# Performance work log

Hardware: AMD Instinct MI355X
Metric: run time of the kernel (lower is better)

## Reference

```python
import jax, jax.numpy as jnp
import numpy as np

D_MODEL = 1024
D_STATE = 16
EXPAND = 2
D_CONV = 4
D_INNER = EXPAND * D_MODEL
BATCH = 1
SEQLEN = 2048


def setup_inputs() -> dict:
    key = jax.random.key(0)
    ks = jax.random.split(key, 8)
    s = 0.02
    x = jax.random.normal(ks[0], (BATCH, SEQLEN, D_MODEL), jnp.float32)
    W_in = jax.random.normal(ks[1], (2 * D_INNER, D_MODEL), jnp.float32) * s
    conv_w = jax.random.normal(ks[2], (D_INNER, 1, D_CONV), jnp.float32) * s
    conv_b = jnp.zeros((D_INNER,), jnp.float32)
    # A_log init as in module: log(arange(1, d_state+1)) tiled over d_inner
    A_log = jnp.log(jnp.tile(jnp.arange(1, D_STATE + 1, dtype=jnp.float32), (D_INNER, 1)))
    D_param = jnp.ones((D_INNER,), jnp.float32)
    W_x = jax.random.normal(ks[3], (2 * D_STATE, D_INNER), jnp.float32) * s
    W_dt = jax.random.normal(ks[4], (D_INNER, D_INNER), jnp.float32) * s
    b_dt = jnp.zeros((D_INNER,), jnp.float32)
    W_out = jax.random.normal(ks[5], (D_MODEL, D_INNER), jnp.float32) * s
    return {"x": x, "W_in": W_in, "conv_w": conv_w, "conv_b": conv_b,
            "A_log": A_log, "D_param": D_param, "W_x": W_x,
            "W_dt": W_dt, "b_dt": b_dt, "W_out": W_out}


def reference(x, W_in, conv_w, conv_b, A_log, D_param, W_x, W_dt, b_dt, W_out):
    B_, L, _ = x.shape
    xz = jnp.einsum('bld,ed->ble', x, W_in)          # [B,L,2*d_inner]
    x_inner, z = jnp.split(xz, 2, axis=-1)
    # causal depthwise conv1d (pad left d_conv-1 == torch pad-both + slice[:L])
    xc = jax.lax.conv_general_dilated(
        jnp.swapaxes(x_inner, 1, 2), conv_w, (1,), [(D_CONV - 1, 0)],
        feature_group_count=D_INNER,
        dimension_numbers=('NCH', 'OIH', 'NCH')) + conv_b[None, :, None]
    x_ssm = jnp.swapaxes(jax.nn.silu(xc), 1, 2)       # [B,L,d_inner]
    dt = jax.nn.softplus(jnp.einsum('ble,fe->blf', x_ssm, W_dt) + b_dt)
    x_dbl = jnp.einsum('ble,se->bls', x_ssm, W_x)     # [B,L,2*d_state]
    B_mat, C_mat = jnp.split(x_dbl, 2, axis=-1)       # each [B,L,d_state]
    A = -jnp.exp(A_log)                               # [d_inner,d_state]
    dA = jnp.exp(dt[..., None] * A)                   # [B,L,d_inner,d_state]
    dBx = B_mat[:, :, None, :] * dt[..., None] * x_ssm[..., None]

    def step(h, inp):
        dA_t, dBx_t, C_t = inp
        h = dA_t * h + dBx_t                          # [B,d_inner,d_state]
        y_t = jnp.einsum('bds,bs->bd', h, C_t)
        return h, y_t

    h0 = jnp.zeros((B_, D_INNER, D_STATE), x.dtype)
    _, ys = jax.lax.scan(step, h0, (jnp.swapaxes(dA, 0, 1),
                                    jnp.swapaxes(dBx, 0, 1),
                                    jnp.swapaxes(C_mat, 0, 1)))
    y = jnp.swapaxes(ys, 0, 1) + D_param * x_ssm      # [B,L,d_inner]
    y = y * jax.nn.silu(z)
    out = jnp.einsum('ble,de->bld', y, W_out)
    return out + x
```

## Files before the change

### kernel.cpp

```cpp
#include <hip/hip_runtime.h>

#define L_SEQ 2048
#define DMODEL 1024
#define DINNER 2048
#define NCHUNK 128
#define TCHUNK 16

typedef __attribute__((ext_vector_type(8))) short bf16x8;
typedef __attribute__((ext_vector_type(4))) float f32x4;

__device__ __forceinline__ float bf2f(unsigned short u) {
  return __uint_as_float(((unsigned)u) << 16);
}
__device__ __forceinline__ unsigned short f2bf(float f) {
  unsigned u = __float_as_uint(f);
  return (unsigned short)((u + 0x7FFFu + ((u >> 16) & 1u)) >> 16);
}
__device__ __forceinline__ void gload_lds16(const void* g, void* l) {
  __builtin_amdgcn_global_load_lds(
      (const __attribute__((address_space(1))) void*)g,
      (__attribute__((address_space(3))) void*)l, 16, 0, 0);
}

__global__ void cvt_f32_bf16(const float4* __restrict__ in, ushort4* __restrict__ out, int n4) {
  int i = blockIdx.x * blockDim.x + threadIdx.x;
  if (i >= n4) return;
  float4 v = in[i];
  ushort4 o;
  o.x = f2bf(v.x); o.y = f2bf(v.y); o.z = f2bf(v.z); o.w = f2bf(v.w);
  out[i] = o;
}

__global__ void zero_bf16(ushort4* __restrict__ out, int n4) {
  int i = blockIdx.x * blockDim.x + threadIdx.x;
  if (i >= n4) return;
  out[i] = ushort4{0, 0, 0, 0};
}

template <int EPI>
__global__ __launch_bounds__(256) void gemm_bt3(
    const unsigned short* __restrict__ A, const unsigned short* __restrict__ B,
    int M, int N, int K, int nx, int ksplit,
    float* __restrict__ outf, unsigned short* __restrict__ outb,
    const float* __restrict__ aux) {
  __shared__ __align__(16) unsigned short As[3 * 128 * 32];
  __shared__ __align__(16) unsigned short Bs[3 * 128 * 32];
  const int tid = threadIdx.x;
  const int lane = tid & 63;
  const int wave = tid >> 6;
  const int wm = wave >> 1, wn = wave & 1;

  const int nwg = gridDim.x;
  const int wg = blockIdx.x;
  const int swzb = (wg & 7) * (nwg >> 3) + (wg >> 3);
  const int tiles = nwg / ksplit;
  const int ks = swzb / tiles;
  const int t = swzb - ks * tiles;
  const int bx = t % nx, by = t / nx;
  const int bm = by * 128, bn = bx * 128;
  const int Ks = K / ksplit;
  const int kbeg = ks * Ks;
  const int nk = Ks >> 5;

  const int srow = tid >> 2, sc4 = tid & 3;
  const int scp = sc4 ^ ((srow >> 1) & 3);
  const unsigned short* Ag = A + (size_t)(bm + srow) * K + scp * 8;
  const unsigned short* Bg = B + (size_t)(bn + srow) * K + scp * 8;
  unsigned short* AsW = &As[srow * 32 + sc4 * 8];
  unsigned short* BsW = &Bs[srow * 32 + sc4 * 8];

  auto STAGE = [&](int buf, int k0) {
    gload_lds16(Ag + k0, AsW + buf * 4096);
    gload_lds16(Ag + (size_t)64 * K + k0, AsW + buf * 4096 + 64 * 32);
    gload_lds16(Bg + k0, BsW + buf * 4096);
    gload_lds16(Bg + (size_t)64 * K + k0, BsW + buf * 4096 + 64 * 32);
  };

  f32x4 acc[4][4] = {};

  const int g = lane >> 4;
  const int r16 = lane & 15;
  const int sw = (g ^ ((r16 >> 1) & 3)) * 8;

  STAGE(0, kbeg);
  STAGE(1, kbeg + 32);
  int cur = 0, stg = 2;

  for (int i = 0; i < nk; ++i) {
    if (i < nk - 1) {
      asm volatile("s_waitcnt vmcnt(4)" ::: "memory");
    } else {
      asm volatile("s_waitcnt vmcnt(0)" ::: "memory");
    }
    __builtin_amdgcn_s_barrier();
    asm volatile("" ::: "memory");
    if (i + 2 < nk) {
      STAGE(stg, kbeg + (i + 2) * 32);
      stg = (stg == 2) ? 0 : stg + 1;
    }

    bf16x8 a[4], b[4];
#pragma unroll
    for (int ii = 0; ii < 4; ++ii)
      a[ii] = *(const bf16x8*)&As[cur * 4096 + (wm * 64 + ii * 16 + r16) * 32 + sw];
#pragma unroll
    for (int j = 0; j < 4; ++j)
      b[j] = *(const bf16x8*)&Bs[cur * 4096 + (wn * 64 + j * 16 + r16) * 32 + sw];
#pragma unroll
    for (int ii = 0; ii < 4; ++ii)
#pragma unroll
      for (int j = 0; j < 4; ++j)
        acc[ii][j] = __builtin_amdgcn_mfma_f32_16x16x32_bf16(a[ii], b[j], acc[ii][j], 0, 0, 0);

    cur = (cur == 2) ? 0 : cur + 1;
  }

  const int rq = lane >> 4;
#pragma unroll
  for (int i = 0; i < 4; ++i)
#pragma unroll
    for (int j = 0; j < 4; ++j)
#pragma unroll
      for (int r = 0; r < 4; ++r) {
        int row = bm + wm * 64 + i * 16 + rq * 4 + r;
        int col = bn + wn * 64 + j * 16 + r16;
        float v = acc[i][j][r];
        if (EPI == 0) {
          outb[(size_t)row * N + col] = f2bf(v);
        } else if (EPI == 3) {
          if (col < 2048) {
            float tt = v + aux[col];
            float sp = (tt > 15.f) ? tt : log1pf(__expf(tt));
            outb[(size_t)row * 2048 + col] = f2bf(sp);
          } else if (col < 2080) {
            outf[(size_t)row * 32 + (col - 2048)] = v;
          }
        } else {
          outf[(size_t)ks * M * N + (size_t)row * N + col] = v;
        }
      }
}

__global__ void reduce_addx(const float4* __restrict__ p, const float4* __restrict__ x,
                            float4* __restrict__ out, int n4) {
  int i = blockIdx.x * 256 + threadIdx.x;
  if (i >= n4) return;
  float4 a = p[i], b = p[n4 + i], c = x[i];
  float4 o;
  o.x = a.x + b.x + c.x; o.y = a.y + b.y + c.y;
  o.z = a.z + b.z + c.z; o.w = a.w + b.w + c.w;
  out[i] = o;
}

__global__ __launch_bounds__(256) void conv_silu8(
    const unsigned short* __restrict__ xz,
    const float* __restrict__ cw, const float* __restrict__ cb,
    unsigned short* __restrict__ x_ssm, unsigned short* __restrict__ sz_out) {
  int idx = blockIdx.x * 256 + threadIdx.x;
  int l = idx >> 8, c0 = (idx & 255) * 8;
  float acc[8];
  float4 b0 = *(const float4*)(cb + c0);
  float4 b1 = *(const float4*)(cb + c0 + 4);
  acc[0] = b0.x; acc[1] = b0.y; acc[2] = b0.z; acc[3] = b0.w;
  acc[4] = b1.x; acc[5] = b1.y; acc[6] = b1.z; acc[7] = b1.w;
  float4 w[8];
#pragma unroll
  for (int j = 0; j < 8; ++j) w[j] = *(const float4*)(cw + (c0 + j) * 4);
#pragma unroll
  for (int k = 0; k < 4; ++k) {
    int lt = l - 3 + k;
    if (lt >= 0) {
      bf16x8 v = *(const bf16x8*)(xz + (size_t)lt * 4096 + c0);
      const float* wk = (const float*)w;
#pragma unroll
      for (int j = 0; j < 8; ++j)
        acc[j] = fmaf(bf2f((unsigned short)v[j]), wk[j * 4 + k], acc[j]);
    }
  }
  bf16x8 zr = *(const bf16x8*)(xz + (size_t)l * 4096 + 2048 + c0);
  bf16x8 ox, oz;
#pragma unroll
  for (int j = 0; j < 8; ++j) {
    float a = acc[j];
    ox[j] = (short)f2bf(a / (1.f + __expf(-a)));
    float zv = bf2f((unsigned short)zr[j]);
    oz[j] = (short)f2bf(zv / (1.f + __expf(-zv)));
  }
  *(bf16x8*)(x_ssm + (size_t)idx * 8) = ox;
  *(bf16x8*)(sz_out + (size_t)idx * 8) = oz;
}

__global__ __launch_bounds__(256) void scan_passA(
    const unsigned short* __restrict__ dtb, const unsigned short* __restrict__ x_ssm,
    const float* __restrict__ x_dbl, const float* __restrict__ A_log,
    float* __restrict__ Pout, float* __restrict__ Hout) {
  int tid = threadIdx.x;
  int c = blockIdx.x & (NCHUNK - 1), db = blockIdx.x >> 7;
  int d = db * 256 + tid;
  int t0 = c * TCHUNK;
  float Av[16];
  const float4* al4 = (const float4*)(A_log + d * 16);
#pragma unroll
  for (int q = 0; q < 4; ++q) {
    float4 a = al4[q];
    Av[q * 4 + 0] = -__expf(a.x); Av[q * 4 + 1] = -__expf(a.y);
    Av[q * 4 + 2] = -__expf(a.z); Av[q * 4 + 3] = -__expf(a.w);
  }
  float h[16];
#pragma unroll
  for (int s = 0; s < 16; ++s) h[s] = 0.f;
  float sum_dt = 0.f;
#pragma unroll 2
  for (int i = 0; i < TCHUNK; ++i) {
    int t = t0 + i;
    float dtv = bf2f(dtb[(size_t)t * 2048 + d]);
    float xv = bf2f(x_ssm[(size_t)t * 2048 + d]);
    float dtx = dtv * xv;
    sum_dt += dtv;
    const float* B = x_dbl + t * 32;
#pragma unroll
    for (int s = 0; s < 16; ++s) {
      float dA = __expf(dtv * Av[s]);
      h[s] = fmaf(dA, h[s], B[s] * dtx);
    }
  }
  float* Ho = Hout + (size_t)c * 32768 + d * 16;
  float* Po = Pout + (size_t)c * 32768 + d * 16;
#pragma unroll
  for (int s = 0; s < 16; ++s) Ho[s] = h[s];
#pragma unroll
  for (int s = 0; s < 16; ++s) Po[s] = __expf(sum_dt * Av[s]);
}

__global__ __launch_bounds__(256) void scan_passB(
    float* __restrict__ P, const float* __restrict__ Hloc) {
  int i = blockIdx.x * 256 + threadIdx.x;
  float h = 0.f;
  for (int c = 0; c < NCHUNK; ++c) {
    size_t o = (size_t)c * 32768 + i;
    float p = P[o];
    float hl = Hloc[o];
    P[o] = h;
    h = fmaf(p, h, hl);
  }
}

__global__ __launch_bounds__(256) void scan_passC(
    const unsigned short* __restrict__ dtb, const unsigned short* __restrict__ x_ssm,
    const float* __restrict__ x_dbl, const float* __restrict__ A_log,
    const float* __restrict__ D_param, const unsigned short* __restrict__ silu_z,
    const float* __restrict__ Hinit, unsigned short* __restrict__ y_out) {
  int tid = threadIdx.x;
  int c = blockIdx.x & (NCHUNK - 1), db = blockIdx.x >> 7;
  int d = db * 256 + tid;
  int t0 = c * TCHUNK;
  float Av[16];
  const float4* al4 = (const float4*)(A_log + d * 16);
#pragma unroll
  for (int q = 0; q < 4; ++q) {
    float4 a = al4[q];
    Av[q * 4 + 0] = -__expf(a.x); Av[q * 4 + 1] = -__expf(a.y);
    Av[q * 4 + 2] = -__expf(a.z); Av[q * 4 + 3] = -__expf(a.w);
  }
  float Dp = D_param[d];
  float h[16];
  const float4* hi4 = (const float4*)(Hinit + (size_t)c * 32768 + d * 16);
#pragma unroll
  for (int q = 0; q < 4; ++q) {
    float4 v = hi4[q];
    h[q * 4 + 0] = v.x; h[q * 4 + 1] = v.y; h[q * 4 + 2] = v.z; h[q * 4 + 3] = v.w;
  }
#pragma unroll 2
  for (int i = 0; i < TCHUNK; ++i) {
    int t = t0 + i;
    float dtv = bf2f(dtb[(size_t)t * 2048 + d]);
    float xv = bf2f(x_ssm[(size_t)t * 2048 + d]);
    float dtx = dtv * xv;
    const float* B = x_dbl + t * 32;
    const float* C = x_dbl + t * 32 + 16;
    float y = 0.f;
#pragma unroll
    for (int s = 0; s < 16; ++s) {
      float dA = __expf(dtv * Av[s]);
      h[s] = fmaf(dA, h[s], B[s] * dtx);
      y = fmaf(h[s], C[s], y);
    }
    float szv = bf2f(silu_z[(size_t)t * 2048 + d]);
    y_out[(size_t)t * 2048 + d] = f2bf((y + Dp * xv) * szv);
  }
}

extern "C" void kernel_launch(void* const* d_in, const int* in_sizes, int n_in,
                              void* d_out, int out_size, void* d_ws, size_t ws_size,
                              hipStream_t stream) {
  const float* x      = (const float*)d_in[0];
  const float* W_in   = (const float*)d_in[1];
  const float* conv_w = (const float*)d_in[2];
  const float* conv_b = (const float*)d_in[3];
  const float* A_log  = (const float*)d_in[4];
  const float* D_par  = (const float*)d_in[5];
  const float* W_x    = (const float*)d_in[6];
  const float* W_dt   = (const float*)d_in[7];
  const float* b_dt   = (const float*)d_in[8];
  const float* W_out  = (const float*)d_in[9];
  float* out = (float*)d_out;

  char* ws = (char*)d_ws;
  unsigned short* xbf    = (unsigned short*)(ws + 0);
  unsigned short* Winbf  = (unsigned short*)(ws + ((size_t)4 << 20));
  unsigned short* Wcomb  = (unsigned short*)(ws + ((size_t)12 << 20));
  unsigned short* Woutbf = (unsigned short*)(ws + ((size_t)21 << 20));
  unsigned short* xz     = (unsigned short*)(ws + ((size_t)25 << 20));
  unsigned short* xssm   = (unsigned short*)(ws + ((size_t)41 << 20));
  unsigned short* siluz  = (unsigned short*)(ws + ((size_t)49 << 20));
  unsigned short* dtb    = (unsigned short*)(ws + ((size_t)57 << 20));
  float* xdbl            = (float*)(ws + ((size_t)65 << 20));
  unsigned short* yfin   = (unsigned short*)(ws + ((size_t)66 << 20));
  float* Pbuf            = (float*)(ws + ((size_t)25 << 20));
  float* Hloc            = (float*)(ws + ((size_t)4 << 20));
  float* part            = (float*)(ws + ((size_t)41 << 20));

  cvt_f32_bf16<<<2048, 256, 0, stream>>>((const float4*)x, (ushort4*)xbf, (L_SEQ * DMODEL) / 4);
  cvt_f32_bf16<<<4096, 256, 0, stream>>>((const float4*)W_in, (ushort4*)Winbf, (2 * DINNER * DMODEL) / 4);
  cvt_f32_bf16<<<4096, 256, 0, stream>>>((const float4*)W_dt, (ushort4*)Wcomb, (DINNER * DINNER) / 4);
  cvt_f32_bf16<<<64, 256, 0, stream>>>((const float4*)W_x, (ushort4*)(Wcomb + (size_t)2048 * 2048),
                                       (32 * DINNER) / 4);
  zero_bf16<<<192, 256, 0, stream>>>((ushort4*)(Wcomb + (size_t)2080 * 2048), (96 * DINNER) / 4);
  cvt_f32_bf16<<<2048, 256, 0, stream>>>((const float4*)W_out, (ushort4*)Woutbf, (DMODEL * DINNER) / 4);

  gemm_bt3<0><<<512, 256, 0, stream>>>(xbf, Winbf, L_SEQ, 4096, DMODEL, 32, 1,
                                       nullptr, xz, nullptr);

  conv_silu8<<<2048, 256, 0, stream>>>(xz, conv_w, conv_b, xssm, siluz);

  gemm_bt3<3><<<272, 256, 0, stream>>>(xssm, Wcomb, L_SEQ, 2176, DINNER, 17, 1,
                                       xdbl, dtb, b_dt);

  scan_passA<<<NCHUNK * (DINNER / 256), 256, 0, stream>>>(dtb, xssm, xdbl, A_log, Pbuf, Hloc);
  scan_passB<<<(DINNER * 16) / 256, 256, 0, stream>>>(Pbuf, Hloc);
  scan_passC<<<NCHUNK * (DINNER / 256), 256, 0, stream>>>(dtb, xssm, xdbl, A_log, D_par, siluz,
                                                          Pbuf, yfin);

  gemm_bt3<4><<<256, 256, 0, stream>>>(yfin, Woutbf, L_SEQ, DMODEL, DINNER, 8, 2,
                                       part, nullptr, nullptr);
  reduce_addx<<<(L_SEQ * DMODEL / 4 + 255) / 256, 256, 0, stream>>>(
      (const float4*)part, (const float4*)x, (float4*)out, L_SEQ * DMODEL / 4);
}
```

Measured before the change: 320.0 us.

## Deepen GEMM K-tile to 64 with 4-stage pipeline and halve scan chunk count

The bf16 GEMM now stages 128x64 K-tiles through a 4-buffer LDS ring with three loads in flight, using an 8-slot XOR swizzle and two MFMA sub-steps per barrier. This halves the number of barriers and waitcnt points per K and deepens prefetch. LDS use grows from 48KB to 128KB per block, which likely limits occupancy to one block per CU. Separately, the chunked scan uses 64 chunks of 32 timesteps instead of 128 of 16, cutting the serial pass-B length and the P/H traffic but giving the parallel passes fewer blocks.

```diff
diff --git a/kernel.cpp b/kernel.cpp
--- a/kernel.cpp
+++ b/kernel.cpp
@@ -3,8 +3,8 @@
 #define L_SEQ 2048
 #define DMODEL 1024
 #define DINNER 2048
-#define NCHUNK 128
-#define TCHUNK 16
+#define NCHUNK 64
+#define TCHUNK 32
 
 typedef __attribute__((ext_vector_type(8))) short bf16x8;
 typedef __attribute__((ext_vector_type(4))) float f32x4;
@@ -38,13 +38,13 @@
 }
 
 template <int EPI>
-__global__ __launch_bounds__(256) void gemm_bt3(
+__global__ __launch_bounds__(256) void gemm_bk64(
     const unsigned short* __restrict__ A, const unsigned short* __restrict__ B,
     int M, int N, int K, int nx, int ksplit,
     float* __restrict__ outf, unsigned short* __restrict__ outb,
     const float* __restrict__ aux) {
-  __shared__ __align__(16) unsigned short As[3 * 128 * 32];
-  __shared__ __align__(16) unsigned short Bs[3 * 128 * 32];
+  __shared__ __align__(16) unsigned short As[4 * 128 * 64];
+  __shared__ __align__(16) unsigned short Bs[4 * 128 * 64];
   const int tid = threadIdx.x;
   const int lane = tid & 63;
   const int wave = tid >> 6;
@@ -60,59 +60,67 @@
   const int bm = by * 128, bn = bx * 128;
   const int Ks = K / ksplit;
   const int kbeg = ks * Ks;
-  const int nk = Ks >> 5;
-
-  const int srow = tid >> 2, sc4 = tid & 3;
-  const int scp = sc4 ^ ((srow >> 1) & 3);
-  const unsigned short* Ag = A + (size_t)(bm + srow) * K + scp * 8;
-  const unsigned short* Bg = B + (size_t)(bn + srow) * K + scp * 8;
-  unsigned short* AsW = &As[srow * 32 + sc4 * 8];
-  unsigned short* BsW = &Bs[srow * 32 + sc4 * 8];
-
-  auto STAGE = [&](int buf, int k0) {
-    gload_lds16(Ag + k0, AsW + buf * 4096);
-    gload_lds16(Ag + (size_t)64 * K + k0, AsW + buf * 4096 + 64 * 32);
-    gload_lds16(Bg + k0, BsW + buf * 4096);
-    gload_lds16(Bg + (size_t)64 * K + k0, BsW + buf * 4096 + 64 * 32);
+  const int nst = Ks >> 6;
+
+  const int srow = wave * 8 + (lane >> 3);
+  const int swslot = (lane & 7) ^ ((lane >> 3) & 7);
+  const unsigned short* Ag = A + (size_t)(bm + srow) * K + kbeg + swslot * 8;
+  const unsigned short* Bg = B + (size_t)(bn + srow) * K + kbeg + swslot * 8;
+
+  auto STAGE = [&](int buf, int kof) {
+#pragma unroll
+    for (int q = 0; q < 4; ++q) {
+      gload_lds16(Ag + (size_t)q * 32 * K + kof, &As[buf * 8192 + (q * 32 + wave * 8) * 64]);
+      gload_lds16(Bg + (size_t)q * 32 * K + kof, &Bs[buf * 8192 + (q * 32 + wave * 8) * 64]);
+    }
   };
 
   f32x4 acc[4][4] = {};
 
   const int g = lane >> 4;
   const int r16 = lane & 15;
-  const int sw = (g ^ ((r16 >> 1) & 3)) * 8;
-
-  STAGE(0, kbeg);
-  STAGE(1, kbeg + 32);
-  int cur = 0, stg = 2;
-
-  for (int i = 0; i < nk; ++i) {
-    if (i < nk - 1) {
-      asm volatile("s_waitcnt vmcnt(4)" ::: "memory");
+  const int rsw = r16 & 7;
+
+  STAGE(0, 0);
+  STAGE(1, 64);
+  STAGE(2, 128);
+  int cur = 0, stg = 3;
+
+  for (int i = 0; i < nst; ++i) {
+    int rem = nst - 1 - i;
+    if (rem >= 2) {
+      asm volatile("s_waitcnt vmcnt(16)" ::: "memory");
+    } else if (rem == 1) {
+      asm volatile("s_waitcnt vmcnt(8)" ::: "memory");
     } else {
       asm volatile("s_waitcnt vmcnt(0)" ::: "memory");
     }
     __builtin_amdgcn_s_barrier();
     asm volatile("" ::: "memory");
-    if (i + 2 < nk) {
-      STAGE(stg, kbeg + (i + 2) * 32);
-      stg = (stg == 2) ? 0 : stg + 1;
-    }
-
-    bf16x8 a[4], b[4];
-#pragma unroll
-    for (int ii = 0; ii < 4; ++ii)
-      a[ii] = *(const bf16x8*)&As[cur * 4096 + (wm * 64 + ii * 16 + r16) * 32 + sw];
-#pragma unroll
-    for (int j = 0; j < 4; ++j)
-      b[j] = *(const bf16x8*)&Bs[cur * 4096 + (wn * 64 + j * 16 + r16) * 32 + sw];
-#pragma unroll
-    for (int ii = 0; ii < 4; ++ii)
+    if (i + 3 < nst) {
+      STAGE(stg, (i + 3) * 64);
+      stg = (stg + 1) & 3;
+    }
+
+#pragma unroll
+    for (int kk = 0; kk < 2; ++kk) {
+      bf16x8 a[4], b[4];
+#pragma unroll
+      for (int ii = 0; ii < 4; ++ii)
+        a[ii] = *(const bf16x8*)&As[cur * 8192 + (wm * 64 + ii * 16 + r16) * 64 +
+                                    ((kk * 4 + g) ^ rsw) * 8];
 #pragma unroll
       for (int j = 0; j < 4; ++j)
-        acc[ii][j] = __builtin_amdgcn_mfma_f32_16x16x32_bf16(a[ii], b[j], acc[ii][j], 0, 0, 0);
-
-    cur = (cur == 2) ? 0 : cur + 1;
+        b[j] = *(const bf16x8*)&Bs[cur * 8192 + (wn * 64 + j * 16 + r16) * 64 +
+                                   ((kk * 4 + g) ^ rsw) * 8];
+#pragma unroll
+      for (int ii = 0; ii < 4; ++ii)
+#pragma unroll
+        for (int j = 0; j < 4; ++j)
+          acc[ii][j] = __builtin_amdgcn_mfma_f32_16x16x32_bf16(a[ii], b[j], acc[ii][j], 0, 0, 0);
+    }
+
+    cur = (cur + 1) & 3;
   }
 
   const int rq = lane >> 4;
@@ -195,7 +203,7 @@
     const float* __restrict__ x_dbl, const float* __restrict__ A_log,
     float* __restrict__ Pout, float* __restrict__ Hout) {
   int tid = threadIdx.x;
-  int c = blockIdx.x & (NCHUNK - 1), db = blockIdx.x >> 7;
+  int c = blockIdx.x & (NCHUNK - 1), db = blockIdx.x / NCHUNK;
   int d = db * 256 + tid;
   int t0 = c * TCHUNK;
   float Av[16];
@@ -251,7 +259,7 @@
     const float* __restrict__ D_param, const unsigned short* __restrict__ silu_z,
     const float* __restrict__ Hinit, unsigned short* __restrict__ y_out) {
   int tid = threadIdx.x;
-  int c = blockIdx.x & (NCHUNK - 1), db = blockIdx.x >> 7;
+  int c = blockIdx.x & (NCHUNK - 1), db = blockIdx.x / NCHUNK;
   int d = db * 256 + tid;
   int t0 = c * TCHUNK;
   float Av[16];
@@ -328,21 +336,21 @@
   zero_bf16<<<192, 256, 0, stream>>>((ushort4*)(Wcomb + (size_t)2080 * 2048), (96 * DINNER) / 4);
   cvt_f32_bf16<<<2048, 256, 0, stream>>>((const float4*)W_out, (ushort4*)Woutbf, (DMODEL * DINNER) / 4);
 
-  gemm_bt3<0><<<512, 256, 0, stream>>>(xbf, Winbf, L_SEQ, 4096, DMODEL, 32, 1,
-                                       nullptr, xz, nullptr);
+  gemm_bk64<0><<<512, 256, 0, stream>>>(xbf, Winbf, L_SEQ, 4096, DMODEL, 32, 1,
+                                        nullptr, xz, nullptr);
 
   conv_silu8<<<2048, 256, 0, stream>>>(xz, conv_w, conv_b, xssm, siluz);
 
-  gemm_bt3<3><<<272, 256, 0, stream>>>(xssm, Wcomb, L_SEQ, 2176, DINNER, 17, 1,
-                                       xdbl, dtb, b_dt);
+  gemm_bk64<3><<<272, 256, 0, stream>>>(xssm, Wcomb, L_SEQ, 2176, DINNER, 17, 1,
+                                        xdbl, dtb, b_dt);
 
   scan_passA<<<NCHUNK * (DINNER / 256), 256, 0, stream>>>(dtb, xssm, xdbl, A_log, Pbuf, Hloc);
   scan_passB<<<(DINNER * 16) / 256, 256, 0, stream>>>(Pbuf, Hloc);
   scan_passC<<<NCHUNK * (DINNER / 256), 256, 0, stream>>>(dtb, xssm, xdbl, A_log, D_par, siluz,
                                                           Pbuf, yfin);
 
-  gemm_bt3<4><<<256, 256, 0, stream>>>(yfin, Woutbf, L_SEQ, DMODEL, DINNER, 8, 2,
-                                       part, nullptr, nullptr);
+  gemm_bk64<4><<<256, 256, 0, stream>>>(yfin, Woutbf, L_SEQ, DMODEL, DINNER, 8, 2,
+                                        part, nullptr, nullptr);
   reduce_addx<<<(L_SEQ * DMODEL / 4 + 255) / 256, 256, 0, stream>>>(
       (const float4*)part, (const float4*)x, (float4*)out, L_SEQ * DMODEL / 4);
 }
```

Measured after the change: 361.1 us. +12.9%, slower.
